# Kernel tuning notes

Measured on AMD Instinct MI355X. Metric: run time of the kernel, lower is better.

Reference implementation:

```python
import jax, jax.numpy as jnp
import numpy as np

B, S, H = 4, 2048, 1024
NH, HD = 16, 64  # num heads, head dim
SCALE = 1.0 / np.sqrt(HD).astype(np.float32)
CLAMP = 1e9
EPS = 1e-9

def setup_inputs() -> dict:
    key = jax.random.key(0)
    ks = jax.random.split(key, 4)
    w_std = 0.02
    return {
        "hidden_states": jax.random.normal(ks[0], (B, S, H), dtype=jnp.float32),
        "Wq": jax.random.normal(ks[1], (H, H), dtype=jnp.float32) * w_std,
        "bq": jnp.zeros((H,), dtype=jnp.float32),
        "Wk": jax.random.normal(ks[2], (H, H), dtype=jnp.float32) * w_std,
        "bk": jnp.zeros((H,), dtype=jnp.float32),
        "Wv": jax.random.normal(ks[3], (H, H), dtype=jnp.float32) * w_std,
        "bv": jnp.zeros((H,), dtype=jnp.float32),
    }

def reference(hidden_states, Wq, bq, Wk, bk, Wv, bv):
    b, s, h = hidden_states.shape
    # linear projections, then split heads: [B,S,H] -> [B,S,NH,HD]
    q = (hidden_states @ Wq + bq).reshape(b, s, NH, HD)
    k = (hidden_states @ Wk + bk).reshape(b, s, NH, HD)
    v = (hidden_states @ Wv + bv).reshape(b, s, NH, HD)
    # scores: [B,NH,Sq,Sk]
    scores = jnp.einsum("bqhd,bkhd->bhqk", q, k) * SCALE
    scores = jnp.clip(scores, -CLAMP, CLAMP)
    probs = jax.nn.softmax(scores, axis=-1) + EPS
    # dropout: eval mode (identity)
    ctx = jnp.einsum("bhqk,bkhd->bqhd", probs, v)
    return ctx.reshape(b, s, h)
```

## Files before the change

kernel.cpp:

```cpp
#include <hip/hip_runtime.h>
#include <hip/hip_bf16.h>
#include <stdint.h>

#define B_ 4
#define S_ 2048
#define H_ 1024
#define NH_ 16
#define HD_ 64
#define SCALE_ 0.125f
#define LOG2E_ 1.4426950408889634f

typedef __bf16 bf16x8 __attribute__((ext_vector_type(8)));
typedef float f32x4 __attribute__((ext_vector_type(4)));
typedef unsigned short us4 __attribute__((ext_vector_type(4)));
typedef unsigned short us8 __attribute__((ext_vector_type(8)));
typedef unsigned short ushort_t;

__device__ __forceinline__ ushort_t f2bf(float f) {
  union { float f; uint32_t u; } a; a.f = f;
  uint32_t r = (a.u + 0x7fffu + ((a.u >> 16) & 1u)) >> 16;
  return (ushort_t)r;
}

__device__ __forceinline__ void async16(const void* g, void* l) {
  __builtin_amdgcn_global_load_lds(
      (const __attribute__((address_space(1))) unsigned int*)(uintptr_t)g,
      (__attribute__((address_space(3))) unsigned int*)(uintptr_t)l, 16, 0, 0);
}

__global__ __launch_bounds__(256) void conv_x(const float4* __restrict__ x,
                                              ushort_t* __restrict__ xb) {
  int i = blockIdx.x * 256 + threadIdx.x;
  float4 v = x[i];
  us4 o;
  o.x = f2bf(v.x); o.y = f2bf(v.y); o.z = f2bf(v.z); o.w = f2bf(v.w);
  *(us4*)(xb + (size_t)i * 4) = o;
}

__global__ __launch_bounds__(256) void conv_w(const float* __restrict__ Wq,
                                              const float* __restrict__ Wk,
                                              const float* __restrict__ Wv,
                                              ushort_t* __restrict__ Wt) {
  __shared__ __align__(16) ushort_t T[64 * 64];
  int bid = blockIdx.x;
  int w = bid >> 8;
  int t2 = bid & 255;
  int kt = (t2 >> 4) * 64, nt = (t2 & 15) * 64;
  const float* W = (w == 0) ? Wq : (w == 1) ? Wk : Wv;
  int tid = threadIdx.x;
  int k = tid >> 2, nq = tid & 3;
#pragma unroll
  for (int j4 = 0; j4 < 4; ++j4) {
    int n = nq * 4 + j4 * 16;
    float4 f = *(const float4*)(W + (size_t)(kt + k) * H_ + nt + n);
    us4 o;
    o.x = f2bf(f.x); o.y = f2bf(f.y); o.z = f2bf(f.z); o.w = f2bf(f.w);
    *(us4*)(T + k * 64 + (((n >> 3) ^ (k & 7)) * 8) + (n & 7)) = o;
  }
  __syncthreads();
  int n2 = tid >> 2, kq = tid & 3;
  us8 o0, o1;
#pragma unroll
  for (int j = 0; j < 16; ++j) {
    int kk = kq * 16 + j;
    ushort_t v = T[kk * 64 + (((n2 >> 3) ^ (kk & 7)) * 8) + (n2 & 7)];
    if (j < 8) o0[j] = v; else o1[j - 8] = v;
  }
  size_t obase = (size_t)w * (H_ * H_) + (size_t)(nt + n2) * H_ + kt + kq * 16;
  *(us8*)(Wt + obase) = o0;
  *(us8*)(Wt + obase + 8) = o1;
}

__global__ __launch_bounds__(256) void qkv_gemm(const ushort_t* __restrict__ Xb,
                                                const ushort_t* __restrict__ Wt,
                                                const float* __restrict__ bq,
                                                const float* __restrict__ bk,
                                                const float* __restrict__ bv,
                                                ushort_t* __restrict__ QKV) {
  __shared__ __align__(16) ushort_t As[128 * 64];
  __shared__ __align__(16) ushort_t Bs[128 * 64];
  int nb = blockIdx.x;
  int mb = blockIdx.y;
  int w = nb >> 3;
  int n_base = (nb & 7) * 128;
  int m_base = mb * 128;
  const ushort_t* Wtw = Wt + (size_t)w * (H_ * H_);
  int tid = threadIdx.x;
  int lane = tid & 63, wave = tid >> 6;
  int wr = wave >> 1, wc = wave & 1;
  int g = lane >> 4, l15 = lane & 15;

  f32x4 acc[4][4];
#pragma unroll
  for (int i = 0; i < 4; i++)
#pragma unroll
    for (int j = 0; j < 4; j++) acc[i][j] = (f32x4){0.f, 0.f, 0.f, 0.f};

  int r0 = tid >> 3, sl = tid & 7;
  int cc = sl ^ (r0 & 7);
  const ushort_t* sA = Xb + (size_t)(m_base + r0) * H_ + cc * 8;
  const ushort_t* sB = Wtw + (size_t)(n_base + r0) * H_ + cc * 8;
  int la = tid * 8;

  for (int kt = 0; kt < 16; ++kt) {
    int k0 = kt * 64;
    __syncthreads();
#pragma unroll
    for (int it = 0; it < 4; ++it) {
      async16(sA + (size_t)it * 32 * H_ + k0, As + la + it * 2048);
      async16(sB + (size_t)it * 32 * H_ + k0, Bs + la + it * 2048);
    }
    __builtin_amdgcn_s_waitcnt(0);
    __syncthreads();

#pragma unroll
    for (int ks = 0; ks < 2; ++ks) {
      bf16x8 af[4], bfr[4];
#pragma unroll
      for (int mi = 0; mi < 4; mi++) {
        int row = wr * 64 + mi * 16 + l15;
        af[mi] = *(const bf16x8*)(As + row * 64 + (((ks * 4 + g) ^ (row & 7)) * 8));
      }
#pragma unroll
      for (int ni = 0; ni < 4; ni++) {
        int row = wc * 64 + ni * 16 + l15;
        bfr[ni] = *(const bf16x8*)(Bs + row * 64 + (((ks * 4 + g) ^ (row & 7)) * 8));
      }
#pragma unroll
      for (int mi = 0; mi < 4; mi++)
#pragma unroll
        for (int ni = 0; ni < 4; ni++)
          acc[mi][ni] = __builtin_amdgcn_mfma_f32_16x16x32_bf16(af[mi], bfr[ni], acc[mi][ni], 0, 0, 0);
    }
  }

  const float* bias = (w == 0) ? bq : (w == 1) ? bk : bv;
  float mult = (w == 0) ? SCALE_ * LOG2E_ : 1.0f;
  if (w == 2) {
    ushort_t* Vout = QKV + 16777216u;
#pragma unroll
    for (int ni = 0; ni < 4; ++ni) {
      int n_col = n_base + wc * 64 + ni * 16 + l15;
      float bb = bias[n_col];
      int hh = n_col >> 6, d = n_col & 63;
#pragma unroll
      for (int mi = 0; mi < 4; ++mi) {
        int m_row = m_base + wr * 64 + mi * 16 + g * 4;
        int bbi = m_row >> 11, s = m_row & 2047;
        us4 o;
#pragma unroll
        for (int reg = 0; reg < 4; ++reg) o[reg] = f2bf(acc[mi][ni][reg] + bb);
        *(us4*)(Vout + ((size_t)((bbi * 16 + hh) * 64 + d)) * 2048 + s) = o;
      }
    }
  } else {
    ushort_t* out = QKV + (size_t)w * (8192u * 1024u);
#pragma unroll
    for (int ni = 0; ni < 4; ++ni) {
      int n_col = n_base + wc * 64 + ni * 16 + l15;
      float bb = bias[n_col];
#pragma unroll
      for (int mi = 0; mi < 4; ++mi) {
        int m_row = m_base + wr * 64 + mi * 16 + g * 4;
#pragma unroll
        for (int reg = 0; reg < 4; ++reg) {
          float v = (acc[mi][ni][reg] + bb) * mult;
          out[(size_t)(m_row + reg) * H_ + n_col] = f2bf(v);
        }
      }
    }
  }
}

__global__ __launch_bounds__(512, 4) void attn(const ushort_t* __restrict__ QKV,
                                               const ushort_t* __restrict__ Vt,
                                               float* __restrict__ out) {
  __shared__ __align__(16) ushort_t Ks[2][64 * 64];
  __shared__ __align__(16) ushort_t Vs[2][64 * 64];
  int qt = blockIdx.x;
  int bh = blockIdx.y;
  int b = bh >> 4, h = bh & 15;
  int tid = threadIdx.x, lane = tid & 63, wave = tid >> 6;
  int g = lane >> 4, l15 = lane & 15;

  const ushort_t* Qb = QKV;
  const ushort_t* Kb = QKV + 8388608u;

  bf16x8 qf[2][2];
#pragma unroll
  for (int mi = 0; mi < 2; ++mi) {
    int q_row = qt * 256 + wave * 32 + mi * 16 + l15;
    size_t qoff = (size_t)(b * S_ + q_row) * H_ + h * HD_;
    qf[mi][0] = *(const bf16x8*)(Qb + qoff + g * 8);
    qf[mi][1] = *(const bf16x8*)(Qb + qoff + 32 + g * 8);
  }

  union { us8 u; bf16x8 v; } ones_u;
#pragma unroll
  for (int i = 0; i < 8; ++i) ones_u.u[i] = 0x3F80;
  bf16x8 onesf = ones_u.v;

  f32x4 of[2][4];
  f32x4 lacc[2];
#pragma unroll
  for (int mi = 0; mi < 2; mi++) {
    lacc[mi] = (f32x4){0.f, 0.f, 0.f, 0.f};
#pragma unroll
    for (int ni = 0; ni < 4; ni++) of[mi][ni] = (f32x4){0.f, 0.f, 0.f, 0.f};
  }

  int ra = (l15 >> 2) * 8 + (l15 & 3);
  int sKa = ((l15 >> 2) & 1) * 4 + (l15 & 3);
  int posK0 = (g ^ sKa) * 8, posK1 = ((4 + g) ^ sKa) * 8;

  int ch = tid;
  int s0 = ch >> 3;
  int cK = (ch & 7) ^ ((((s0 >> 3) & 1) << 2) | (s0 & 3));
  int cV = (ch & 7) ^ (s0 & 7);
  const ushort_t* srcK = Kb + (size_t)(b * S_ + s0) * H_ + h * HD_ + cK * 8;
  const ushort_t* srcV = Vt + ((size_t)bh * 64 + s0) * S_ + cV * 8;

  async16(srcK, Ks[0] + ch * 8);
  async16(srcV, Vs[0] + ch * 8);

  for (int kb = 0; kb < 32; ++kb) {
    int cur = kb & 1, nxt = cur ^ 1;
    __syncthreads();
    if (kb < 31) {
      async16(srcK + (size_t)(kb + 1) * 64 * H_, Ks[nxt] + ch * 8);
      async16(srcV + (size_t)(kb + 1) * 64, Vs[nxt] + ch * 8);
      __builtin_amdgcn_s_waitcnt(0xF72);
    } else {
      __builtin_amdgcn_s_waitcnt(0xF70);
    }
    __syncthreads();
    const ushort_t* Kc = Ks[cur];
    const ushort_t* Vc = Vs[cur];

#pragma unroll
    for (int kk = 0; kk < 2; ++kk) {
      int rowa = kk * 32 + ra;
      int rowb = rowa + 4;
      bf16x8 ka0 = *(const bf16x8*)(Kc + rowa * 64 + posK0);
      bf16x8 ka1 = *(const bf16x8*)(Kc + rowa * 64 + posK1);
      bf16x8 kb0 = *(const bf16x8*)(Kc + rowb * 64 + posK0);
      bf16x8 kb1 = *(const bf16x8*)(Kc + rowb * 64 + posK1);
      bf16x8 vf[4];
#pragma unroll
      for (int ni = 0; ni < 4; ++ni) {
        int row = ni * 16 + l15;
        vf[ni] = *(const bf16x8*)(Vc + row * 64 + (((kk * 4 + g) ^ (row & 7)) * 8));
      }
#pragma unroll
      for (int mi = 0; mi < 2; ++mi) {
        f32x4 sa = (f32x4){0.f, 0.f, 0.f, 0.f};
        f32x4 sb = (f32x4){0.f, 0.f, 0.f, 0.f};
        sa = __builtin_amdgcn_mfma_f32_16x16x32_bf16(ka0, qf[mi][0], sa, 0, 0, 0);
        sa = __builtin_amdgcn_mfma_f32_16x16x32_bf16(ka1, qf[mi][1], sa, 0, 0, 0);
        sb = __builtin_amdgcn_mfma_f32_16x16x32_bf16(kb0, qf[mi][0], sb, 0, 0, 0);
        sb = __builtin_amdgcn_mfma_f32_16x16x32_bf16(kb1, qf[mi][1], sb, 0, 0, 0);
        float pa0 = __builtin_amdgcn_exp2f(sa[0]);
        float pa1 = __builtin_amdgcn_exp2f(sa[1]);
        float pa2 = __builtin_amdgcn_exp2f(sa[2]);
        float pa3 = __builtin_amdgcn_exp2f(sa[3]);
        float pb0 = __builtin_amdgcn_exp2f(sb[0]);
        float pb1 = __builtin_amdgcn_exp2f(sb[1]);
        float pb2 = __builtin_amdgcn_exp2f(sb[2]);
        float pb3 = __builtin_amdgcn_exp2f(sb[3]);
        union { bf16x8 v; unsigned int u[4]; } pf;
        pf.u[0] = __builtin_amdgcn_perm(__float_as_uint(pa1) + 0x8000u,
                                        __float_as_uint(pa0) + 0x8000u, 0x07060302u);
        pf.u[1] = __builtin_amdgcn_perm(__float_as_uint(pa3) + 0x8000u,
                                        __float_as_uint(pa2) + 0x8000u, 0x07060302u);
        pf.u[2] = __builtin_amdgcn_perm(__float_as_uint(pb1) + 0x8000u,
                                        __float_as_uint(pb0) + 0x8000u, 0x07060302u);
        pf.u[3] = __builtin_amdgcn_perm(__float_as_uint(pb3) + 0x8000u,
                                        __float_as_uint(pb2) + 0x8000u, 0x07060302u);
#pragma unroll
        for (int ni = 0; ni < 4; ++ni)
          of[mi][ni] = __builtin_amdgcn_mfma_f32_16x16x32_bf16(vf[ni], pf.v, of[mi][ni], 0, 0, 0);
        lacc[mi] = __builtin_amdgcn_mfma_f32_16x16x32_bf16(onesf, pf.v, lacc[mi], 0, 0, 0);
      }
    }
  }

#pragma unroll
  for (int mi = 0; mi < 2; ++mi) {
    float inv = 1.0f / lacc[mi][0];
    int qglob = qt * 256 + wave * 32 + mi * 16 + l15;
    float* obase = out + (size_t)(b * S_ + qglob) * H_ + h * HD_ + g * 4;
#pragma unroll
    for (int ni = 0; ni < 4; ++ni) {
      float4 vv;
      vv.x = of[mi][ni][0] * inv;
      vv.y = of[mi][ni][1] * inv;
      vv.z = of[mi][ni][2] * inv;
      vv.w = of[mi][ni][3] * inv;
      *(float4*)(obase + ni * 16) = vv;
    }
  }
}

extern "C" void kernel_launch(void* const* d_in, const int* in_sizes, int n_in,
                              void* d_out, int out_size, void* d_ws, size_t ws_size,
                              hipStream_t stream) {
  const float* hs = (const float*)d_in[0];
  const float* Wq = (const float*)d_in[1];
  const float* bq = (const float*)d_in[2];
  const float* Wk = (const float*)d_in[3];
  const float* bk = (const float*)d_in[4];
  const float* Wv = (const float*)d_in[5];
  const float* bv = (const float*)d_in[6];
  float* out = (float*)d_out;

  ushort_t* Xb  = (ushort_t*)d_ws;
  ushort_t* Wt  = Xb + 8388608u;
  ushort_t* QKV = Wt + 3145728u;
  ushort_t* Vtp = QKV + 16777216u;

  conv_x<<<8192, 256, 0, stream>>>((const float4*)hs, Xb);
  conv_w<<<768, 256, 0, stream>>>(Wq, Wk, Wv, Wt);
  qkv_gemm<<<dim3(24, 64), 256, 0, stream>>>(Xb, Wt, bq, bk, bv, QKV);
  attn<<<dim3(8, 64), 512, 0, stream>>>(QKV, Vtp, out);
}
```

Before: 243.2 us.

## Double-buffer QKV GEMM LDS tiles and use raw s_barrier in attention loop

The QKV projection GEMM now keeps two LDS buffers for the A and B tiles. It prefetches the next K-slice with async global-to-LDS loads while MFMAs run on the current slice, so global latency is hidden instead of stalling on waitcnt(0) every iteration. This doubles the GEMM's LDS footprint to 64KB, which can lower occupancy. Separately, __syncthreads in the attention loop is replaced with a bare s_barrier, which avoids the compiler-inserted waitcnt/fences and relies on the explicit vmcnt waits for correctness.

```diff
diff --git a/kernel.cpp b/kernel.cpp
--- a/kernel.cpp
+++ b/kernel.cpp
@@ -26,6 +26,10 @@
   __builtin_amdgcn_global_load_lds(
       (const __attribute__((address_space(1))) unsigned int*)(uintptr_t)g,
       (__attribute__((address_space(3))) unsigned int*)(uintptr_t)l, 16, 0, 0);
+}
+
+__device__ __forceinline__ void raw_barrier() {
+  asm volatile("s_barrier" ::: "memory");
 }
 
 __global__ __launch_bounds__(256) void conv_x(const float4* __restrict__ x,
@@ -77,8 +81,10 @@
                                                 const float* __restrict__ bk,
                                                 const float* __restrict__ bv,
                                                 ushort_t* __restrict__ QKV) {
-  __shared__ __align__(16) ushort_t As[128 * 64];
-  __shared__ __align__(16) ushort_t Bs[128 * 64];
+  __shared__ __align__(16) ushort_t As0[128 * 64];
+  __shared__ __align__(16) ushort_t As1[128 * 64];
+  __shared__ __align__(16) ushort_t Bs0[128 * 64];
+  __shared__ __align__(16) ushort_t Bs1[128 * 64];
   int nb = blockIdx.x;
   int mb = blockIdx.y;
   int w = nb >> 3;
@@ -102,16 +108,27 @@
   const ushort_t* sB = Wtw + (size_t)(n_base + r0) * H_ + cc * 8;
   int la = tid * 8;
 
+#pragma unroll
+  for (int it = 0; it < 4; ++it) {
+    async16(sA + (size_t)it * 32 * H_, As0 + la + it * 2048);
+    async16(sB + (size_t)it * 32 * H_, Bs0 + la + it * 2048);
+  }
+  __builtin_amdgcn_s_waitcnt(0xF70);
+  raw_barrier();
+
   for (int kt = 0; kt < 16; ++kt) {
-    int k0 = kt * 64;
-    __syncthreads();
-#pragma unroll
-    for (int it = 0; it < 4; ++it) {
-      async16(sA + (size_t)it * 32 * H_ + k0, As + la + it * 2048);
-      async16(sB + (size_t)it * 32 * H_ + k0, Bs + la + it * 2048);
-    }
-    __builtin_amdgcn_s_waitcnt(0);
-    __syncthreads();
+    const ushort_t* Ac = (kt & 1) ? As1 : As0;
+    const ushort_t* Bc = (kt & 1) ? Bs1 : Bs0;
+    ushort_t* An = (kt & 1) ? As0 : As1;
+    ushort_t* Bn = (kt & 1) ? Bs0 : Bs1;
+    if (kt < 15) {
+      int k0 = (kt + 1) * 64;
+#pragma unroll
+      for (int it = 0; it < 4; ++it) {
+        async16(sA + (size_t)it * 32 * H_ + k0, An + la + it * 2048);
+        async16(sB + (size_t)it * 32 * H_ + k0, Bn + la + it * 2048);
+      }
+    }
 
 #pragma unroll
     for (int ks = 0; ks < 2; ++ks) {
@@ -119,18 +136,23 @@
 #pragma unroll
       for (int mi = 0; mi < 4; mi++) {
         int row = wr * 64 + mi * 16 + l15;
-        af[mi] = *(const bf16x8*)(As + row * 64 + (((ks * 4 + g) ^ (row & 7)) * 8));
+        af[mi] = *(const bf16x8*)(Ac + row * 64 + (((ks * 4 + g) ^ (row & 7)) * 8));
       }
 #pragma unroll
       for (int ni = 0; ni < 4; ni++) {
         int row = wc * 64 + ni * 16 + l15;
-        bfr[ni] = *(const bf16x8*)(Bs + row * 64 + (((ks * 4 + g) ^ (row & 7)) * 8));
+        bfr[ni] = *(const bf16x8*)(Bc + row * 64 + (((ks * 4 + g) ^ (row & 7)) * 8));
       }
 #pragma unroll
       for (int mi = 0; mi < 4; mi++)
 #pragma unroll
         for (int ni = 0; ni < 4; ni++)
           acc[mi][ni] = __builtin_amdgcn_mfma_f32_16x16x32_bf16(af[mi], bfr[ni], acc[mi][ni], 0, 0, 0);
+    }
+
+    if (kt < 15) {
+      __builtin_amdgcn_s_waitcnt(0xF70);
+      raw_barrier();
     }
   }
 
@@ -225,7 +247,7 @@
 
   for (int kb = 0; kb < 32; ++kb) {
     int cur = kb & 1, nxt = cur ^ 1;
-    __syncthreads();
+    raw_barrier();
     if (kb < 31) {
       async16(srcK + (size_t)(kb + 1) * 64 * H_, Ks[nxt] + ch * 8);
       async16(srcV + (size_t)(kb + 1) * 64, Vs[nxt] + ch * 8);
@@ -233,7 +255,7 @@
     } else {
       __builtin_amdgcn_s_waitcnt(0xF70);
     }
-    __syncthreads();
+    raw_barrier();
     const ushort_t* Kc = Ks[cur];
     const ushort_t* Vc = Vs[cur];
 
```

Measured after the change: 234.9 us. 3.4% less time.
